# Kernel tuning notes

Hardware: AMD Instinct MI355X
Metric: run time of the kernel (lower is better)

The kernel has to match this reference:

```python
import math
import jax, jax.numpy as jnp
import numpy as np

NUM_HEADS = 8
ALPHA = 20.0
LN_EPS = 1e-5


def setup_inputs() -> dict:
    key = jax.random.key(0)
    ks = jax.random.split(key, 6)
    B, N, C = 8, 4096, 512
    s = 1.0 / math.sqrt(C)
    return {
        "x": jax.random.normal(ks[0], (B, N, C), dtype=jnp.float32),
        "qkv_w": jax.random.normal(ks[1], (C, 3 * C), dtype=jnp.float32) * s,
        "qkv_b": jnp.zeros((3 * C,), dtype=jnp.float32),
        "ln_g": jnp.ones((C,), dtype=jnp.float32),
        "ln_b": jnp.zeros((C,), dtype=jnp.float32),
        "out_w": jax.random.normal(ks[2], (C, C), dtype=jnp.float32) * s,
        "out_b": jnp.zeros((C,), dtype=jnp.float32),
    }


def _forward(x, qkv_w, qkv_b, ln_g, ln_b, out_w, out_b):
    B, N, C = x.shape
    H = NUM_HEADS
    D = C // H
    qkv = x @ qkv_w + qkv_b  # (B,N,3C)
    q, k, v = jnp.split(qkv, 3, axis=-1)

    def to_heads(t):
        return t.reshape(B, N, H, D).transpose(0, 2, 1, 3)  # (B,H,N,D)

    q, k, v = to_heads(q), to_heads(k), to_heads(v)

    # cosine-inhibit feature maps
    q_norm = jnp.linalg.norm(q, axis=-1, keepdims=True)  # (B,H,N,1)
    k_norm = jnp.linalg.norm(k, axis=-1, keepdims=True)
    q_t = q / q_norm
    dq = jnp.tanh(q / q_norm * ALPHA) * (math.pi / 4)
    dk = jnp.tanh(k / k_norm * ALPHA) * (math.pi / 4)
    k3 = jnp.abs(k) ** 3
    kf = jnp.concatenate([k3 * jnp.cos(dk), k3 * jnp.sin(dk)], axis=-1)  # (B,H,N,2D)
    power = 1.5 * (0.5 + jnp.tanh(q_norm))
    q_t = (q_t ** 2) ** power
    qf = jnp.concatenate([q_t * jnp.cos(dq), q_t * jnp.sin(dq)], axis=-1)  # (B,H,N,2D)

    # O(N) linear attention
    k_mean = jnp.mean(kf, axis=2, keepdims=True)  # (B,H,1,2D)
    z = 1.0 / (jnp.einsum('bhnf,bhmf->bhnm', qf, k_mean) + 1e-6)  # (B,H,N,1)
    scale = N ** (-0.5)
    kv = jnp.einsum('bhnf,bhnd->bhfd', kf * scale, v * scale)  # (B,H,2D,D)
    out = jnp.einsum('bhnf,bhfd->bhnd', qf, kv) * z  # (B,H,N,D)

    out = out.transpose(0, 2, 1, 3).reshape(B, N, C)
    # LayerNorm
    mu = jnp.mean(out, axis=-1, keepdims=True)
    var = jnp.var(out, axis=-1, keepdims=True)
    out = (out - mu) * jax.lax.rsqrt(var + LN_EPS) * ln_g + ln_b
    return out @ out_w + out_b


def reference(x, qkv_w, qkv_b, ln_g, ln_b, out_w, out_b):
    return _forward(x, qkv_w, qkv_b, ln_g, ln_b, out_w, out_b)
```

## Files before the change

### kernel.cpp

```cpp
#include <hip/hip_runtime.h>
#include <math.h>

#define Bb 8
#define Nn 4096
#define Cc 512
#define Hh 8
#define Dd 64
#define Ff 128
#define M_ROWS (Bb * Nn)
#define PI4f 0.78539816339744830962f
#define CHB 16
#define PART 8320

using bf16x8 = __attribute__((ext_vector_type(8))) short;
using f32x4 = __attribute__((ext_vector_type(4))) float;

__device__ __forceinline__ unsigned short f2bf(float f) {
  unsigned u = __float_as_uint(f);
  u += 0x7FFFu + ((u >> 16) & 1u);
  return (unsigned short)(u >> 16);
}
__device__ __forceinline__ float bf2f(unsigned short h) {
  return __uint_as_float(((unsigned)h) << 16);
}
__device__ __forceinline__ float grp16_sum(float v) {
  v += __shfl_xor(v, 1);
  v += __shfl_xor(v, 2);
  v += __shfl_xor(v, 4);
  v += __shfl_xor(v, 8);
  return v;
}
__device__ __forceinline__ float wsum64(float v) {
#pragma unroll
  for (int m = 32; m >= 1; m >>= 1) v += __shfl_xor(v, m, 64);
  return v;
}
__device__ __forceinline__ float fast_tanh(float x) {
  float e = __expf(2.0f * x);
  return 1.0f - 2.0f / (e + 1.0f);
}

__global__ __launch_bounds__(256) void x_convert(const float* __restrict__ x,
                                                 unsigned short* __restrict__ xb) {
  size_t i = ((size_t)blockIdx.x * 256 + threadIdx.x) * 8;
  float4 a = *(const float4*)(x + i);
  float4 b = *(const float4*)(x + i + 4);
  int4 o;
  o.x = (int)f2bf(a.x) | ((int)f2bf(a.y) << 16);
  o.y = (int)f2bf(a.z) | ((int)f2bf(a.w) << 16);
  o.z = (int)f2bf(b.x) | ((int)f2bf(b.y) << 16);
  o.w = (int)f2bf(b.z) | ((int)f2bf(b.w) << 16);
  *(int4*)(xb + i) = o;
}

__global__ __launch_bounds__(256) void w_transpose(const float* __restrict__ qkvw,
                                                   const float* __restrict__ outw,
                                                   unsigned short* __restrict__ wt,
                                                   unsigned short* __restrict__ owt) {
  __shared__ float tile[64][65];
  const int bid = blockIdx.x;
  const float* src;
  unsigned short* dst;
  int ldsrc, j0, k0;
  if (bid < 192) {
    src = qkvw; dst = wt; ldsrc = 1536;
    j0 = (bid % 24) * 64; k0 = (bid / 24) * 64;
  } else {
    int r = bid - 192;
    src = outw; dst = owt; ldsrc = 512;
    j0 = (r & 7) * 64; k0 = (r >> 3) * 64;
  }
  const int t = threadIdx.x;
  const int rr = t >> 4, cc = (t & 15) * 4;
#pragma unroll
  for (int it = 0; it < 4; ++it) {
    float4 v = *(const float4*)(src + (size_t)(k0 + rr + it * 16) * ldsrc + j0 + cc);
    tile[rr + it * 16][cc + 0] = v.x;
    tile[rr + it * 16][cc + 1] = v.y;
    tile[rr + it * 16][cc + 2] = v.z;
    tile[rr + it * 16][cc + 3] = v.w;
  }
  __syncthreads();
  const int j = t >> 2, kq = (t & 3) * 16;
  unsigned short u[16];
#pragma unroll
  for (int p = 0; p < 16; ++p) u[p] = f2bf(tile[kq + p][j]);
  int4 o;
  o.x = (int)u[0] | ((int)u[1] << 16);
  o.y = (int)u[2] | ((int)u[3] << 16);
  o.z = (int)u[4] | ((int)u[5] << 16);
  o.w = (int)u[6] | ((int)u[7] << 16);
  int4 o2;
  o2.x = (int)u[8] | ((int)u[9] << 16);
  o2.y = (int)u[10] | ((int)u[11] << 16);
  o2.z = (int)u[12] | ((int)u[13] << 16);
  o2.w = (int)u[14] | ((int)u[15] << 16);
  *(int4*)(dst + (size_t)(j0 + j) * 512 + k0 + kq) = o;
  *(int4*)(dst + (size_t)(j0 + j) * 512 + k0 + kq + 8) = o2;
}

__global__ __launch_bounds__(256) void kv_kernel(const unsigned short* __restrict__ xb,
                                                 const unsigned short* __restrict__ wt,
                                                 const float* __restrict__ qkvb,
                                                 float* __restrict__ part) {
  __shared__ char smraw[54272];
  unsigned short* As = (unsigned short*)smraw;
  unsigned short* Bs = As + 128 * 72;
  unsigned short* kf_t = (unsigned short*)smraw;
  unsigned short* v_t = kf_t + 128 * 136;
  float* ksl = (float*)(smraw + 52224);
  const int t = threadIdx.x, lane = t & 63, wv = t >> 6;
  const int i = lane & 15, g = lane >> 4, kq = g * 8;
  const int bh = blockIdx.x >> 4, chunk = blockIdx.x & 15;
  const int b = bh >> 3, h = bh & 7;
  const int sr = t >> 1, sko = (t & 1) * 32;
  const int wrow = (sr < 64) ? (512 + h * 64 + sr) : (1024 + h * 64 + sr - 64);
  const unsigned short* bg = wt + (size_t)wrow * 512 + sko;
  float bias_[8];
#pragma unroll
  for (int ni = 0; ni < 4; ++ni) bias_[ni] = qkvb[512 + h * 64 + 16 * ni + i];
#pragma unroll
  for (int ni = 4; ni < 8; ++ni) bias_[ni] = qkvb[1024 + h * 64 + 16 * (ni - 4) + i];
  f32x4 kvf[2][4] = {};
  float ksc[4] = {0.f, 0.f, 0.f, 0.f}, kss[4] = {0.f, 0.f, 0.f, 0.f};
  const size_t rowbase = (size_t)b * Nn + chunk * 256;
  const unsigned short* ag0 = xb + (rowbase + sr) * 512 + sko;
  bf16x8 pa[4], pb[4];
#pragma unroll
  for (int p = 0; p < 4; ++p) {
    pa[p] = *(const bf16x8*)(ag0 + p * 8);
    pb[p] = *(const bf16x8*)(bg + p * 8);
  }
  for (int t2 = 0; t2 < 2; ++t2) {
    const unsigned short* ag = xb + (rowbase + t2 * 128 + sr) * 512 + sko;
    f32x4 acc[2][8] = {};
    for (int k0 = 0; k0 < 512; k0 += 64) {
      __syncthreads();
#pragma unroll
      for (int p = 0; p < 4; ++p) {
        *(bf16x8*)&As[sr * 72 + sko + p * 8] = pa[p];
        *(bf16x8*)&Bs[sr * 72 + sko + p * 8] = pb[p];
      }
      __syncthreads();
      if (k0 < 448) {
#pragma unroll
        for (int p = 0; p < 4; ++p) {
          pa[p] = *(const bf16x8*)(ag + k0 + 64 + p * 8);
          pb[p] = *(const bf16x8*)(bg + k0 + 64 + p * 8);
        }
      } else if (t2 == 0) {
        const unsigned short* ag1 = ag + 128 * 512;
#pragma unroll
        for (int p = 0; p < 4; ++p) {
          pa[p] = *(const bf16x8*)(ag1 + p * 8);
          pb[p] = *(const bf16x8*)(bg + p * 8);
        }
      }
#pragma unroll
      for (int ks = 0; ks < 2; ++ks) {
        bf16x8 am[2], bn[8];
#pragma unroll
        for (int mi = 0; mi < 2; ++mi)
          am[mi] = *(const bf16x8*)&As[(32 * wv + 16 * mi + i) * 72 + ks * 32 + kq];
#pragma unroll
        for (int ni = 0; ni < 8; ++ni)
          bn[ni] = *(const bf16x8*)&Bs[(16 * ni + i) * 72 + ks * 32 + kq];
#pragma unroll
        for (int mi = 0; mi < 2; ++mi)
#pragma unroll
          for (int ni = 0; ni < 8; ++ni)
            acc[mi][ni] = __builtin_amdgcn_mfma_f32_16x16x32_bf16(am[mi], bn[ni], acc[mi][ni], 0, 0, 0);
      }
    }
    __syncthreads();
#pragma unroll
    for (int mi = 0; mi < 2; ++mi) {
      float nrm[4];
#pragma unroll
      for (int r = 0; r < 4; ++r) {
        float s = 0.f;
#pragma unroll
        for (int ni = 0; ni < 4; ++ni) {
          float kx = acc[mi][ni][r] + bias_[ni];
          s += kx * kx;
        }
        nrm[r] = sqrtf(grp16_sum(s));
      }
#pragma unroll
      for (int ni = 0; ni < 4; ++ni)
#pragma unroll
        for (int r = 0; r < 4; ++r) {
          float kx = acc[mi][ni][r] + bias_[ni];
          float dk = fast_tanh(kx / nrm[r] * 20.0f) * PI4f;
          float a3 = fabsf(kx);
          a3 = a3 * a3 * a3;
          float sn, cs;
          __sincosf(dk, &sn, &cs);
          float kc = a3 * cs, ksn = a3 * sn;
          ksc[ni] += kc;
          kss[ni] += ksn;
          const int nl = 32 * wv + 16 * mi + 4 * g + r;
          kf_t[(16 * ni + i) * 136 + nl] = f2bf(kc);
          kf_t[(64 + 16 * ni + i) * 136 + nl] = f2bf(ksn);
        }
#pragma unroll
      for (int ni = 4; ni < 8; ++ni)
#pragma unroll
        for (int r = 0; r < 4; ++r) {
          const int nl = 32 * wv + 16 * mi + 4 * g + r;
          v_t[(16 * (ni - 4) + i) * 136 + nl] = f2bf(acc[mi][ni][r] + bias_[ni]);
        }
    }
    __syncthreads();
#pragma unroll
    for (int ks2 = 0; ks2 < 4; ++ks2) {
      bf16x8 a2[2], b2[4];
#pragma unroll
      for (int mi = 0; mi < 2; ++mi)
        a2[mi] = *(const bf16x8*)&kf_t[(32 * wv + 16 * mi + i) * 136 + ks2 * 32 + kq];
#pragma unroll
      for (int ni = 0; ni < 4; ++ni)
        b2[ni] = *(const bf16x8*)&v_t[(16 * ni + i) * 136 + ks2 * 32 + kq];
#pragma unroll
      for (int mi = 0; mi < 2; ++mi)
#pragma unroll
        for (int ni = 0; ni < 4; ++ni)
          kvf[mi][ni] = __builtin_amdgcn_mfma_f32_16x16x32_bf16(a2[mi], b2[ni], kvf[mi][ni], 0, 0, 0);
    }
  }
  float* pw = part + (size_t)blockIdx.x * PART;
#pragma unroll
  for (int mi = 0; mi < 2; ++mi)
#pragma unroll
    for (int ni = 0; ni < 4; ++ni)
#pragma unroll
      for (int r = 0; r < 4; ++r)
        pw[(32 * wv + 16 * mi + 4 * g + r) * 64 + 16 * ni + i] = kvf[mi][ni][r];
#pragma unroll
  for (int ni = 0; ni < 4; ++ni) {
    float c = ksc[ni];
    c += __shfl_xor(c, 16);
    c += __shfl_xor(c, 32);
    float s = kss[ni];
    s += __shfl_xor(s, 16);
    s += __shfl_xor(s, 32);
    if (lane < 16) {
      ksl[wv * 128 + 16 * ni + lane] = c;
      ksl[wv * 128 + 64 + 16 * ni + lane] = s;
    }
  }
  __syncthreads();
  if (t < 128) pw[8192 + t] = ksl[t] + ksl[128 + t] + ksl[256 + t] + ksl[384 + t];
}

__global__ __launch_bounds__(256) void kv_reduce(const float* __restrict__ part,
                                                 unsigned short* __restrict__ kvt,
                                                 float* __restrict__ kmean) {
  const int bh = blockIdx.x;
  const float invN = 1.0f / Nn;
  const size_t base = (size_t)bh * CHB * PART;
  for (int idx = threadIdx.x; idx < 8192; idx += 256) {
    float s = 0.f;
#pragma unroll
    for (int c = 0; c < CHB; ++c) s += part[base + (size_t)c * PART + idx];
    int f = idx >> 6, d = idx & 63;
    kvt[(size_t)bh * 8192 + d * 128 + f] = f2bf(s * invN);
  }
  if (threadIdx.x < 128) {
    float s = 0.f;
#pragma unroll
    for (int c = 0; c < CHB; ++c) s += part[base + (size_t)c * PART + 8192 + threadIdx.x];
    kmean[bh * 128 + threadIdx.x] = s * invN;
  }
}

__global__ __launch_bounds__(256) void attn_kernel(const unsigned short* __restrict__ xb,
                                                   const unsigned short* __restrict__ wt,
                                                   const float* __restrict__ qkvb,
                                                   const unsigned short* __restrict__ kvt,
                                                   const float* __restrict__ kmean,
                                                   unsigned short* __restrict__ attb) {
  __shared__ char smraw[52736];
  unsigned short* As = (unsigned short*)smraw;
  unsigned short* Bs = As + 128 * 72;
  unsigned short* qf_t = (unsigned short*)smraw;
  unsigned short* kv_s = (unsigned short*)(smraw + 34816);
  float* km = (float*)(smraw + 34816 + 17408);
  const int t = threadIdx.x, lane = t & 63, wv = t >> 6;
  const int i = lane & 15, g = lane >> 4, kq = g * 8;
  const int bh = blockIdx.x >> 5, chunk = blockIdx.x & 31;
  const int b = bh >> 3, h = bh & 7;
  const size_t row0 = (size_t)b * Nn + chunk * 128;
  if (t < 128) km[t] = kmean[bh * 128 + t];
  {
    const unsigned short* src = kvt + (size_t)bh * 8192;
#pragma unroll
    for (int it = 0; it < 4; ++it) {
      int idx = t + it * 256;
      int d = idx >> 4, f8 = (idx & 15) * 8;
      *(bf16x8*)&kv_s[d * 136 + f8] = *(const bf16x8*)(src + d * 128 + f8);
    }
  }
  const int sr = t >> 1, sko = (t & 1) * 32;
  const int c2 = t >> 2, ko2 = (t & 3) * 16;
  const unsigned short* ag = xb + (row0 + sr) * 512 + sko;
  const unsigned short* bgq = wt + (size_t)(h * 64 + c2) * 512 + ko2;
  bf16x8 pa[4], pb[2];
#pragma unroll
  for (int p = 0; p < 4; ++p) pa[p] = *(const bf16x8*)(ag + p * 8);
#pragma unroll
  for (int p = 0; p < 2; ++p) pb[p] = *(const bf16x8*)(bgq + p * 8);
  f32x4 acc[2][4] = {};
  for (int k0 = 0; k0 < 512; k0 += 64) {
    __syncthreads();
#pragma unroll
    for (int p = 0; p < 4; ++p) *(bf16x8*)&As[sr * 72 + sko + p * 8] = pa[p];
#pragma unroll
    for (int p = 0; p < 2; ++p) *(bf16x8*)&Bs[c2 * 72 + ko2 + p * 8] = pb[p];
    __syncthreads();
    if (k0 < 448) {
#pragma unroll
      for (int p = 0; p < 4; ++p) pa[p] = *(const bf16x8*)(ag + k0 + 64 + p * 8);
#pragma unroll
      for (int p = 0; p < 2; ++p) pb[p] = *(const bf16x8*)(bgq + k0 + 64 + p * 8);
    }
#pragma unroll
    for (int ks = 0; ks < 2; ++ks) {
      bf16x8 am[2], bn[4];
#pragma unroll
      for (int mi = 0; mi < 2; ++mi)
        am[mi] = *(const bf16x8*)&As[(32 * wv + 16 * mi + i) * 72 + ks * 32 + kq];
#pragma unroll
      for (int ni = 0; ni < 4; ++ni)
        bn[ni] = *(const bf16x8*)&Bs[(16 * ni + i) * 72 + ks * 32 + kq];
#pragma unroll
      for (int mi = 0; mi < 2; ++mi)
#pragma unroll
        for (int ni = 0; ni < 4; ++ni)
          acc[mi][ni] = __builtin_amdgcn_mfma_f32_16x16x32_bf16(am[mi], bn[ni], acc[mi][ni], 0, 0, 0);
    }
  }
  __syncthreads();
  float bqv[4];
#pragma unroll
  for (int ni = 0; ni < 4; ++ni) bqv[ni] = qkvb[h * 64 + 16 * ni + i];
  float z[2][4];
#pragma unroll
  for (int mi = 0; mi < 2; ++mi) {
    float nrm[4];
#pragma unroll
    for (int r = 0; r < 4; ++r) {
      float s = 0.f;
#pragma unroll
      for (int ni = 0; ni < 4; ++ni) {
        float q = acc[mi][ni][r] + bqv[ni];
        s += q * q;
      }
      nrm[r] = sqrtf(grp16_sum(s));
    }
#pragma unroll
    for (int r = 0; r < 4; ++r) {
      float pwr = 1.5f * (0.5f + fast_tanh(nrm[r]));
      float dp = 0.f;
      const int nl = 32 * wv + 16 * mi + 4 * g + r;
#pragma unroll
      for (int ni = 0; ni < 4; ++ni) {
        float q = acc[mi][ni][r] + bqv[ni];
        float qt = q / nrm[r];
        float dq = fast_tanh(qt * 20.0f) * PI4f;
        float qtp = exp2f(pwr * __log2f(qt * qt));
        float sn, cs;
        __sincosf(dq, &sn, &cs);
        float qc = qtp * cs, qs = qtp * sn;
        dp += qc * km[16 * ni + i] + qs * km[64 + 16 * ni + i];
        qf_t[nl * 136 + 16 * ni + i] = f2bf(qc);
        qf_t[nl * 136 + 64 + 16 * ni + i] = f2bf(qs);
      }
      z[mi][r] = 1.0f / (grp16_sum(dp) + 1e-6f);
    }
  }
  __syncthreads();
  f32x4 pacc[2][4] = {};
#pragma unroll
  for (int ks2 = 0; ks2 < 4; ++ks2) {
    bf16x8 a2[2], b2[4];
#pragma unroll
    for (int mi = 0; mi < 2; ++mi)
      a2[mi] = *(const bf16x8*)&qf_t[(32 * wv + 16 * mi + i) * 136 + ks2 * 32 + kq];
#pragma unroll
    for (int ni = 0; ni < 4; ++ni)
      b2[ni] = *(const bf16x8*)&kv_s[(16 * ni + i) * 136 + ks2 * 32 + kq];
#pragma unroll
    for (int mi = 0; mi < 2; ++mi)
#pragma unroll
      for (int ni = 0; ni < 4; ++ni)
        pacc[mi][ni] = __builtin_amdgcn_mfma_f32_16x16x32_bf16(a2[mi], b2[ni], pacc[mi][ni], 0, 0, 0);
  }
#pragma unroll
  for (int mi = 0; mi < 2; ++mi)
#pragma unroll
    for (int ni = 0; ni < 4; ++ni)
#pragma unroll
      for (int r = 0; r < 4; ++r)
        attb[(row0 + 32 * wv + 16 * mi + 4 * g + r) * 512 + h * 64 + 16 * ni + i] =
            f2bf(pacc[mi][ni][r] * z[mi][r]);
}

__global__ __launch_bounds__(256) void ln_kernel(unsigned short* __restrict__ attb,
                                                 const float* __restrict__ gg,
                                                 const float* __restrict__ bb) {
  const int lane = threadIdx.x & 63, wv = threadIdx.x >> 6;
  const size_t row = (size_t)blockIdx.x * 4 + wv;
  unsigned short* p = attb + row * 512 + lane * 8;
  bf16x8 v = *(bf16x8*)p;
  float x[8];
#pragma unroll
  for (int j = 0; j < 8; ++j) x[j] = bf2f((unsigned short)v[j]);
  float s = 0.f;
#pragma unroll
  for (int j = 0; j < 8; ++j) s += x[j];
  const float mu = wsum64(s) * (1.0f / 512.0f);
  float sq = 0.f;
#pragma unroll
  for (int j = 0; j < 8; ++j) {
    float d = x[j] - mu;
    sq += d * d;
  }
  const float rstd = rsqrtf(wsum64(sq) * (1.0f / 512.0f) + 1e-5f);
  const float4 g0 = *(const float4*)(gg + lane * 8);
  const float4 g1 = *(const float4*)(gg + lane * 8 + 4);
  const float4 b0 = *(const float4*)(bb + lane * 8);
  const float4 b1 = *(const float4*)(bb + lane * 8 + 4);
  float gv[8] = {g0.x, g0.y, g0.z, g0.w, g1.x, g1.y, g1.z, g1.w};
  float bv[8] = {b0.x, b0.y, b0.z, b0.w, b1.x, b1.y, b1.z, b1.w};
#pragma unroll
  for (int j = 0; j < 8; ++j)
    v[j] = (short)f2bf((x[j] - mu) * rstd * gv[j] + bv[j]);
  *(bf16x8*)p = v;
}

__global__ __launch_bounds__(256) void out_gemm(const unsigned short* __restrict__ attb,
                                                const unsigned short* __restrict__ owt,
                                                const float* __restrict__ ob,
                                                float* __restrict__ outp) {
  __shared__ unsigned short As[128 * 72];
  __shared__ unsigned short Bs[128 * 72];
  const int t = threadIdx.x, lane = t & 63, wv = t >> 6;
  const int i = lane & 15, g = lane >> 4, kq = g * 8;
  const int wm = wv >> 1, wn = wv & 1;
  const int m0 = (blockIdx.x >> 2) * 128, n0 = (blockIdx.x & 3) * 128;
  const int sr = t >> 1, sko = (t & 1) * 32;
  const unsigned short* ag = attb + (size_t)(m0 + sr) * 512 + sko;
  const unsigned short* bg = owt + (size_t)(n0 + sr) * 512 + sko;
  f32x4 acc[4][4] = {};
  bf16x8 pa[4], pb[4];
#pragma unroll
  for (int p = 0; p < 4; ++p) {
    pa[p] = *(const bf16x8*)(ag + p * 8);
    pb[p] = *(const bf16x8*)(bg + p * 8);
  }
  for (int k0 = 0; k0 < 512; k0 += 64) {
    __syncthreads();
#pragma unroll
    for (int p = 0; p < 4; ++p) {
      *(bf16x8*)&As[sr * 72 + sko + p * 8] = pa[p];
      *(bf16x8*)&Bs[sr * 72 + sko + p * 8] = pb[p];
    }
    __syncthreads();
    if (k0 < 448) {
#pragma unroll
      for (int p = 0; p < 4; ++p) {
        pa[p] = *(const bf16x8*)(ag + k0 + 64 + p * 8);
        pb[p] = *(const bf16x8*)(bg + k0 + 64 + p * 8);
      }
    }
#pragma unroll
    for (int ks = 0; ks < 2; ++ks) {
      bf16x8 am[4], bn[4];
#pragma unroll
      for (int q = 0; q < 4; ++q) {
        am[q] = *(const bf16x8*)&As[(64 * wm + 16 * q + i) * 72 + ks * 32 + kq];
        bn[q] = *(const bf16x8*)&Bs[(64 * wn + 16 * q + i) * 72 + ks * 32 + kq];
      }
#pragma unroll
      for (int mi = 0; mi < 4; ++mi)
#pragma unroll
        for (int ni = 0; ni < 4; ++ni)
          acc[mi][ni] = __builtin_amdgcn_mfma_f32_16x16x32_bf16(am[mi], bn[ni], acc[mi][ni], 0, 0, 0);
    }
  }
#pragma unroll
  for (int ni = 0; ni < 4; ++ni) {
    float bv = ob[n0 + 64 * wn + 16 * ni + i];
#pragma unroll
    for (int mi = 0; mi < 4; ++mi)
#pragma unroll
      for (int r = 0; r < 4; ++r)
        outp[(size_t)(m0 + 64 * wm + 16 * mi + 4 * g + r) * 512 + n0 + 64 * wn +
             16 * ni + i] = acc[mi][ni][r] + bv;
  }
}

extern "C" void kernel_launch(void* const* d_in, const int* in_sizes, int n_in,
                              void* d_out, int out_size, void* d_ws,
                              size_t ws_size, hipStream_t stream) {
  const float* x = (const float*)d_in[0];
  const float* qkv_w = (const float*)d_in[1];
  const float* qkv_b = (const float*)d_in[2];
  const float* ln_g = (const float*)d_in[3];
  const float* ln_b = (const float*)d_in[4];
  const float* out_w = (const float*)d_in[5];
  const float* out_b = (const float*)d_in[6];
  float* out = (float*)d_out;

  char* w = (char*)d_ws;
  unsigned short* xb = (unsigned short*)w;
  unsigned short* wt = (unsigned short*)(w + 33554432);
  unsigned short* owt = (unsigned short*)(w + 35127296);
  unsigned short* kvt = (unsigned short*)(w + 35651584);
  float* kmean = (float*)(w + 36700160);
  char* R = w + 36732928;
  float* part = (float*)R;
  unsigned short* attb = (unsigned short*)R;

  x_convert<<<8192, 256, 0, stream>>>(x, xb);
  w_transpose<<<256, 256, 0, stream>>>(qkv_w, out_w, wt, owt);
  kv_kernel<<<1024, 256, 0, stream>>>(xb, wt, qkv_b, part);
  kv_reduce<<<64, 256, 0, stream>>>(part, kvt, kmean);
  attn_kernel<<<2048, 256, 0, stream>>>(xb, wt, qkv_b, kvt, kmean, attb);
  ln_kernel<<<8192, 256, 0, stream>>>(attb, ln_g, ln_b);
  out_gemm<<<1024, 256, 0, stream>>>(attb, owt, out_b, out);
}
```

Baseline: 357.8 us.

## Split QKV projection into standalone GEMM, use LDS direct loads and atomic KV reduction

Replaces the fused kv_kernel and attn_kernel, which each recomputed their share of the QKV projection, with one large qkv_gemm that writes a bf16 QKV buffer. The feature kernels then read from that buffer. The partial-sum buffer and kv_reduce kernel are dropped in favour of float atomicAdd into a zeroed accumulator. Both GEMMs switch to global_load_lds direct-to-LDS loads with an XCD-aware block swizzle. The cost is an extra round trip through a 100 MB bf16 intermediate, a memset, and loss of register prefetch double-buffering.

Measured after the change: 353.9 us. About the same (-1.1%).

```diff
diff --git a/kernel.cpp b/kernel.cpp
--- a/kernel.cpp
+++ b/kernel.cpp
@@ -5,12 +5,7 @@
 #define Nn 4096
 #define Cc 512
 #define Hh 8
-#define Dd 64
-#define Ff 128
-#define M_ROWS (Bb * Nn)
 #define PI4f 0.78539816339744830962f
-#define CHB 16
-#define PART 8320
 
 using bf16x8 = __attribute__((ext_vector_type(8))) short;
 using f32x4 = __attribute__((ext_vector_type(4))) float;
@@ -38,6 +33,11 @@
 __device__ __forceinline__ float fast_tanh(float x) {
   float e = __expf(2.0f * x);
   return 1.0f - 2.0f / (e + 1.0f);
+}
+__device__ __forceinline__ void gload16(const unsigned short* g, unsigned short* l) {
+  __builtin_amdgcn_global_load_lds(
+      (const __attribute__((address_space(1))) void*)g,
+      (__attribute__((address_space(3))) void*)l, 16, 0, 0);
 }
 
 __global__ __launch_bounds__(256) void x_convert(const float* __restrict__ x,
@@ -99,100 +99,101 @@
   *(int4*)(dst + (size_t)(j0 + j) * 512 + k0 + kq + 8) = o2;
 }
 
-__global__ __launch_bounds__(256) void kv_kernel(const unsigned short* __restrict__ xb,
-                                                 const unsigned short* __restrict__ wt,
-                                                 const float* __restrict__ qkvb,
-                                                 float* __restrict__ part) {
-  __shared__ char smraw[54272];
-  unsigned short* As = (unsigned short*)smraw;
-  unsigned short* Bs = As + 128 * 72;
-  unsigned short* kf_t = (unsigned short*)smraw;
-  unsigned short* v_t = kf_t + 128 * 136;
-  float* ksl = (float*)(smraw + 52224);
+__global__ __launch_bounds__(256) void qkv_gemm(const unsigned short* __restrict__ xb,
+                                                const unsigned short* __restrict__ wt,
+                                                const float* __restrict__ bias,
+                                                unsigned short* __restrict__ qkvb) {
+  __shared__ unsigned short As[128 * 64];
+  __shared__ unsigned short Bs[128 * 64];
   const int t = threadIdx.x, lane = t & 63, wv = t >> 6;
   const int i = lane & 15, g = lane >> 4, kq = g * 8;
-  const int bh = blockIdx.x >> 4, chunk = blockIdx.x & 15;
+  const int wm = wv >> 1, wn = wv & 1;
+  const int sbid = ((int)blockIdx.x & 7) * 384 + ((int)blockIdx.x >> 3);
+  const int mt = sbid / 12, nt = sbid - mt * 12;
+  const int m0 = mt * 128, n0 = nt * 128;
+  const int lrow = lane >> 3, lchunk = (lane & 7) * 8;
+  const unsigned short* agb = xb + (size_t)(m0 + 32 * wv + lrow) * 512 + lchunk;
+  const unsigned short* bgb = wt + (size_t)(n0 + 32 * wv + lrow) * 512 + lchunk;
+  unsigned short* asb = &As[(32 * wv) * 64];
+  unsigned short* bsb = &Bs[(32 * wv) * 64];
+  f32x4 acc[4][4] = {};
+  for (int k0 = 0; k0 < 512; k0 += 64) {
+    __syncthreads();
+#pragma unroll
+    for (int c = 0; c < 4; ++c) {
+      gload16(agb + (size_t)(8 * c) * 512 + k0, asb + 8 * c * 64);
+      gload16(bgb + (size_t)(8 * c) * 512 + k0, bsb + 8 * c * 64);
+    }
+    __syncthreads();
+#pragma unroll
+    for (int ks = 0; ks < 2; ++ks) {
+      bf16x8 am[4], bn[4];
+#pragma unroll
+      for (int q = 0; q < 4; ++q) {
+        am[q] = *(const bf16x8*)&As[(64 * wm + 16 * q + i) * 64 + ks * 32 + kq];
+        bn[q] = *(const bf16x8*)&Bs[(64 * wn + 16 * q + i) * 64 + ks * 32 + kq];
+      }
+#pragma unroll
+      for (int mi = 0; mi < 4; ++mi)
+#pragma unroll
+        for (int ni = 0; ni < 4; ++ni)
+          acc[mi][ni] = __builtin_amdgcn_mfma_f32_16x16x32_bf16(am[mi], bn[ni], acc[mi][ni], 0, 0, 0);
+    }
+  }
+#pragma unroll
+  for (int ni = 0; ni < 4; ++ni) {
+    const int col = n0 + 64 * wn + 16 * ni + i;
+    const float bv = bias[col];
+#pragma unroll
+    for (int mi = 0; mi < 4; ++mi) {
+      const size_t rowb = (size_t)(m0 + 64 * wm + 16 * mi + 4 * g) * 1536 + col;
+#pragma unroll
+      for (int r = 0; r < 4; ++r)
+        qkvb[rowb + (size_t)r * 1536] = f2bf(acc[mi][ni][r] + bv);
+    }
+  }
+}
+
+__global__ __launch_bounds__(256) void kv_feat(const unsigned short* __restrict__ qkvb,
+                                               float* __restrict__ kvacc,
+                                               float* __restrict__ ksum) {
+  __shared__ unsigned short kf_t[128 * 136];
+  __shared__ unsigned short v_t[64 * 136];
+  const int t = threadIdx.x, lane = t & 63, wv = t >> 6;
+  const int i = lane & 15, g = lane >> 4, kq = g * 8;
+  const int bh = (int)blockIdx.x >> 4, chunk = (int)blockIdx.x & 15;
   const int b = bh >> 3, h = bh & 7;
-  const int sr = t >> 1, sko = (t & 1) * 32;
-  const int wrow = (sr < 64) ? (512 + h * 64 + sr) : (1024 + h * 64 + sr - 64);
-  const unsigned short* bg = wt + (size_t)wrow * 512 + sko;
-  float bias_[8];
-#pragma unroll
-  for (int ni = 0; ni < 4; ++ni) bias_[ni] = qkvb[512 + h * 64 + 16 * ni + i];
-#pragma unroll
-  for (int ni = 4; ni < 8; ++ni) bias_[ni] = qkvb[1024 + h * 64 + 16 * (ni - 4) + i];
+  const size_t rowbase = (size_t)b * Nn + chunk * 256;
   f32x4 kvf[2][4] = {};
   float ksc[4] = {0.f, 0.f, 0.f, 0.f}, kss[4] = {0.f, 0.f, 0.f, 0.f};
-  const size_t rowbase = (size_t)b * Nn + chunk * 256;
-  const unsigned short* ag0 = xb + (rowbase + sr) * 512 + sko;
-  bf16x8 pa[4], pb[4];
-#pragma unroll
-  for (int p = 0; p < 4; ++p) {
-    pa[p] = *(const bf16x8*)(ag0 + p * 8);
-    pb[p] = *(const bf16x8*)(bg + p * 8);
-  }
   for (int t2 = 0; t2 < 2; ++t2) {
-    const unsigned short* ag = xb + (rowbase + t2 * 128 + sr) * 512 + sko;
-    f32x4 acc[2][8] = {};
-    for (int k0 = 0; k0 < 512; k0 += 64) {
-      __syncthreads();
-#pragma unroll
-      for (int p = 0; p < 4; ++p) {
-        *(bf16x8*)&As[sr * 72 + sko + p * 8] = pa[p];
-        *(bf16x8*)&Bs[sr * 72 + sko + p * 8] = pb[p];
-      }
-      __syncthreads();
-      if (k0 < 448) {
-#pragma unroll
-        for (int p = 0; p < 4; ++p) {
-          pa[p] = *(const bf16x8*)(ag + k0 + 64 + p * 8);
-          pb[p] = *(const bf16x8*)(bg + k0 + 64 + p * 8);
-        }
-      } else if (t2 == 0) {
-        const unsigned short* ag1 = ag + 128 * 512;
-#pragma unroll
-        for (int p = 0; p < 4; ++p) {
-          pa[p] = *(const bf16x8*)(ag1 + p * 8);
-          pb[p] = *(const bf16x8*)(bg + p * 8);
+#pragma unroll
+    for (int mi = 0; mi < 2; ++mi) {
+      float kx[4][4], vx[4][4];
+#pragma unroll
+      for (int r = 0; r < 4; ++r) {
+        const unsigned short* rp =
+            qkvb + (rowbase + t2 * 128 + 32 * wv + 16 * mi + 4 * g + r) * 1536 + h * 64 + i;
+#pragma unroll
+        for (int ni = 0; ni < 4; ++ni) {
+          kx[ni][r] = bf2f(rp[512 + 16 * ni]);
+          vx[ni][r] = bf2f(rp[1024 + 16 * ni]);
         }
       }
-#pragma unroll
-      for (int ks = 0; ks < 2; ++ks) {
-        bf16x8 am[2], bn[8];
-#pragma unroll
-        for (int mi = 0; mi < 2; ++mi)
-          am[mi] = *(const bf16x8*)&As[(32 * wv + 16 * mi + i) * 72 + ks * 32 + kq];
-#pragma unroll
-        for (int ni = 0; ni < 8; ++ni)
-          bn[ni] = *(const bf16x8*)&Bs[(16 * ni + i) * 72 + ks * 32 + kq];
-#pragma unroll
-        for (int mi = 0; mi < 2; ++mi)
-#pragma unroll
-          for (int ni = 0; ni < 8; ++ni)
-            acc[mi][ni] = __builtin_amdgcn_mfma_f32_16x16x32_bf16(am[mi], bn[ni], acc[mi][ni], 0, 0, 0);
-      }
-    }
-    __syncthreads();
-#pragma unroll
-    for (int mi = 0; mi < 2; ++mi) {
       float nrm[4];
 #pragma unroll
       for (int r = 0; r < 4; ++r) {
-        float s = 0.f;
-#pragma unroll
-        for (int ni = 0; ni < 4; ++ni) {
-          float kx = acc[mi][ni][r] + bias_[ni];
-          s += kx * kx;
-        }
+        float s = kx[0][r] * kx[0][r] + kx[1][r] * kx[1][r] +
+                  kx[2][r] * kx[2][r] + kx[3][r] * kx[3][r];
         nrm[r] = sqrtf(grp16_sum(s));
       }
 #pragma unroll
       for (int ni = 0; ni < 4; ++ni)
 #pragma unroll
         for (int r = 0; r < 4; ++r) {
-          float kx = acc[mi][ni][r] + bias_[ni];
-          float dk = fast_tanh(kx / nrm[r] * 20.0f) * PI4f;
-          float a3 = fabsf(kx);
+          float k1 = kx[ni][r];
+          float dk = fast_tanh(k1 / nrm[r] * 20.0f) * PI4f;
+          float a3 = fabsf(k1);
           a3 = a3 * a3 * a3;
           float sn, cs;
           __sincosf(dk, &sn, &cs);
@@ -202,13 +203,7 @@
           const int nl = 32 * wv + 16 * mi + 4 * g + r;
           kf_t[(16 * ni + i) * 136 + nl] = f2bf(kc);
           kf_t[(64 + 16 * ni + i) * 136 + nl] = f2bf(ksn);
-        }
-#pragma unroll
-      for (int ni = 4; ni < 8; ++ni)
-#pragma unroll
-        for (int r = 0; r < 4; ++r) {
-          const int nl = 32 * wv + 16 * mi + 4 * g + r;
-          v_t[(16 * (ni - 4) + i) * 136 + nl] = f2bf(acc[mi][ni][r] + bias_[ni]);
+          v_t[(16 * ni + i) * 136 + nl] = f2bf(vx[ni][r]);
         }
     }
     __syncthreads();
@@ -227,15 +222,17 @@
         for (int ni = 0; ni < 4; ++ni)
           kvf[mi][ni] = __builtin_amdgcn_mfma_f32_16x16x32_bf16(a2[mi], b2[ni], kvf[mi][ni], 0, 0, 0);
     }
-  }
-  float* pw = part + (size_t)blockIdx.x * PART;
+    __syncthreads();
+  }
 #pragma unroll
   for (int mi = 0; mi < 2; ++mi)
 #pragma unroll
     for (int ni = 0; ni < 4; ++ni)
 #pragma unroll
       for (int r = 0; r < 4; ++r)
-        pw[(32 * wv + 16 * mi + 4 * g + r) * 64 + 16 * ni + i] = kvf[mi][ni][r];
+        atomicAdd(kvacc + (size_t)bh * 8192 +
+                      (32 * wv + 16 * mi + 4 * g + r) * 64 + 16 * ni + i,
+                  kvf[mi][ni][r]);
 #pragma unroll
   for (int ni = 0; ni < 4; ++ni) {
     float c = ksc[ni];
@@ -245,117 +242,49 @@
     s += __shfl_xor(s, 16);
     s += __shfl_xor(s, 32);
     if (lane < 16) {
-      ksl[wv * 128 + 16 * ni + lane] = c;
-      ksl[wv * 128 + 64 + 16 * ni + lane] = s;
-    }
-  }
-  __syncthreads();
-  if (t < 128) pw[8192 + t] = ksl[t] + ksl[128 + t] + ksl[256 + t] + ksl[384 + t];
-}
-
-__global__ __launch_bounds__(256) void kv_reduce(const float* __restrict__ part,
-                                                 unsigned short* __restrict__ kvt,
-                                                 float* __restrict__ kmean) {
-  const int bh = blockIdx.x;
-  const float invN = 1.0f / Nn;
-  const size_t base = (size_t)bh * CHB * PART;
-  for (int idx = threadIdx.x; idx < 8192; idx += 256) {
-    float s = 0.f;
-#pragma unroll
-    for (int c = 0; c < CHB; ++c) s += part[base + (size_t)c * PART + idx];
-    int f = idx >> 6, d = idx & 63;
-    kvt[(size_t)bh * 8192 + d * 128 + f] = f2bf(s * invN);
-  }
-  if (threadIdx.x < 128) {
-    float s = 0.f;
-#pragma unroll
-    for (int c = 0; c < CHB; ++c) s += part[base + (size_t)c * PART + 8192 + threadIdx.x];
-    kmean[bh * 128 + threadIdx.x] = s * invN;
-  }
-}
-
-__global__ __launch_bounds__(256) void attn_kernel(const unsigned short* __restrict__ xb,
-                                                   const unsigned short* __restrict__ wt,
-                                                   const float* __restrict__ qkvb,
-                                                   const unsigned short* __restrict__ kvt,
-                                                   const float* __restrict__ kmean,
-                                                   unsigned short* __restrict__ attb) {
-  __shared__ char smraw[52736];
-  unsigned short* As = (unsigned short*)smraw;
-  unsigned short* Bs = As + 128 * 72;
-  unsigned short* qf_t = (unsigned short*)smraw;
-  unsigned short* kv_s = (unsigned short*)(smraw + 34816);
-  float* km = (float*)(smraw + 34816 + 17408);
+      atomicAdd(ksum + bh * 128 + 16 * ni + lane, c);
+      atomicAdd(ksum + bh * 128 + 64 + 16 * ni + lane, s);
+    }
+  }
+}
+
+__global__ __launch_bounds__(256) void attn_feat(const unsigned short* __restrict__ qkvb,
+                                                 const float* __restrict__ kvacc,
+                                                 const float* __restrict__ ksum,
+                                                 unsigned short* __restrict__ attb) {
+  __shared__ unsigned short qf_t[128 * 136];
+  __shared__ unsigned short kv_s[64 * 136];
+  __shared__ float km[128];
   const int t = threadIdx.x, lane = t & 63, wv = t >> 6;
   const int i = lane & 15, g = lane >> 4, kq = g * 8;
-  const int bh = blockIdx.x >> 5, chunk = blockIdx.x & 31;
+  const int bh = (int)blockIdx.x >> 5, chunk = (int)blockIdx.x & 31;
   const int b = bh >> 3, h = bh & 7;
   const size_t row0 = (size_t)b * Nn + chunk * 128;
-  if (t < 128) km[t] = kmean[bh * 128 + t];
-  {
-    const unsigned short* src = kvt + (size_t)bh * 8192;
-#pragma unroll
-    for (int it = 0; it < 4; ++it) {
-      int idx = t + it * 256;
-      int d = idx >> 4, f8 = (idx & 15) * 8;
-      *(bf16x8*)&kv_s[d * 136 + f8] = *(const bf16x8*)(src + d * 128 + f8);
-    }
-  }
-  const int sr = t >> 1, sko = (t & 1) * 32;
-  const int c2 = t >> 2, ko2 = (t & 3) * 16;
-  const unsigned short* ag = xb + (row0 + sr) * 512 + sko;
-  const unsigned short* bgq = wt + (size_t)(h * 64 + c2) * 512 + ko2;
-  bf16x8 pa[4], pb[2];
-#pragma unroll
-  for (int p = 0; p < 4; ++p) pa[p] = *(const bf16x8*)(ag + p * 8);
-#pragma unroll
-  for (int p = 0; p < 2; ++p) pb[p] = *(const bf16x8*)(bgq + p * 8);
-  f32x4 acc[2][4] = {};
-  for (int k0 = 0; k0 < 512; k0 += 64) {
-    __syncthreads();
-#pragma unroll
-    for (int p = 0; p < 4; ++p) *(bf16x8*)&As[sr * 72 + sko + p * 8] = pa[p];
-#pragma unroll
-    for (int p = 0; p < 2; ++p) *(bf16x8*)&Bs[c2 * 72 + ko2 + p * 8] = pb[p];
-    __syncthreads();
-    if (k0 < 448) {
-#pragma unroll
-      for (int p = 0; p < 4; ++p) pa[p] = *(const bf16x8*)(ag + k0 + 64 + p * 8);
-#pragma unroll
-      for (int p = 0; p < 2; ++p) pb[p] = *(const bf16x8*)(bgq + k0 + 64 + p * 8);
-    }
-#pragma unroll
-    for (int ks = 0; ks < 2; ++ks) {
-      bf16x8 am[2], bn[4];
-#pragma unroll
-      for (int mi = 0; mi < 2; ++mi)
-        am[mi] = *(const bf16x8*)&As[(32 * wv + 16 * mi + i) * 72 + ks * 32 + kq];
-#pragma unroll
-      for (int ni = 0; ni < 4; ++ni)
-        bn[ni] = *(const bf16x8*)&Bs[(16 * ni + i) * 72 + ks * 32 + kq];
-#pragma unroll
-      for (int mi = 0; mi < 2; ++mi)
-#pragma unroll
-        for (int ni = 0; ni < 4; ++ni)
-          acc[mi][ni] = __builtin_amdgcn_mfma_f32_16x16x32_bf16(am[mi], bn[ni], acc[mi][ni], 0, 0, 0);
-    }
-  }
+  const float invN = 1.0f / Nn;
+  for (int idx = t; idx < 8192; idx += 256) {
+    int f = idx >> 6, d = idx & 63;
+    kv_s[d * 136 + f] = f2bf(kvacc[(size_t)bh * 8192 + idx] * invN);
+  }
+  if (t < 128) km[t] = ksum[bh * 128 + t] * invN;
+  float qx[2][4][4];
+#pragma unroll
+  for (int mi = 0; mi < 2; ++mi)
+#pragma unroll
+    for (int r = 0; r < 4; ++r) {
+      const unsigned short* rp =
+          qkvb + (row0 + 32 * wv + 16 * mi + 4 * g + r) * 1536 + h * 64 + i;
+#pragma unroll
+      for (int ni = 0; ni < 4; ++ni) qx[mi][ni][r] = bf2f(rp[16 * ni]);
+    }
   __syncthreads();
-  float bqv[4];
-#pragma unroll
-  for (int ni = 0; ni < 4; ++ni) bqv[ni] = qkvb[h * 64 + 16 * ni + i];
   float z[2][4];
 #pragma unroll
   for (int mi = 0; mi < 2; ++mi) {
     float nrm[4];
 #pragma unroll
     for (int r = 0; r < 4; ++r) {
-      float s = 0.f;
-#pragma unroll
-      for (int ni = 0; ni < 4; ++ni) {
-        float q = acc[mi][ni][r] + bqv[ni];
-        s += q * q;
-      }
+      float s = qx[mi][0][r] * qx[mi][0][r] + qx[mi][1][r] * qx[mi][1][r] +
+                qx[mi][2][r] * qx[mi][2][r] + qx[mi][3][r] * qx[mi][3][r];
       nrm[r] = sqrtf(grp16_sum(s));
     }
 #pragma unroll
@@ -365,7 +294,7 @@
       const int nl = 32 * wv + 16 * mi + 4 * g + r;
 #pragma unroll
       for (int ni = 0; ni < 4; ++ni) {
-        float q = acc[mi][ni][r] + bqv[ni];
+        float q = qx[mi][ni][r];
         float qt = q / nrm[r];
         float dq = fast_tanh(qt * 20.0f) * PI4f;
         float qtp = exp2f(pwr * __log2f(qt * qt));
@@ -443,44 +372,34 @@
                                                 const unsigned short* __restrict__ owt,
                                                 const float* __restrict__ ob,
                                                 float* __restrict__ outp) {
-  __shared__ unsigned short As[128 * 72];
-  __shared__ unsigned short Bs[128 * 72];
+  __shared__ unsigned short As[128 * 64];
+  __shared__ unsigned short Bs[128 * 64];
   const int t = threadIdx.x, lane = t & 63, wv = t >> 6;
   const int i = lane & 15, g = lane >> 4, kq = g * 8;
   const int wm = wv >> 1, wn = wv & 1;
-  const int m0 = (blockIdx.x >> 2) * 128, n0 = (blockIdx.x & 3) * 128;
-  const int sr = t >> 1, sko = (t & 1) * 32;
-  const unsigned short* ag = attb + (size_t)(m0 + sr) * 512 + sko;
-  const unsigned short* bg = owt + (size_t)(n0 + sr) * 512 + sko;
+  const int sbid = ((int)blockIdx.x & 7) * 128 + ((int)blockIdx.x >> 3);
+  const int m0 = (sbid >> 2) * 128, n0 = (sbid & 3) * 128;
+  const int lrow = lane >> 3, lchunk = (lane & 7) * 8;
+  const unsigned short* agb = attb + (size_t)(m0 + 32 * wv + lrow) * 512 + lchunk;
+  const unsigned short* bgb = owt + (size_t)(n0 + 32 * wv + lrow) * 512 + lchunk;
+  unsigned short* asb = &As[(32 * wv) * 64];
+  unsigned short* bsb = &Bs[(32 * wv) * 64];
   f32x4 acc[4][4] = {};
-  bf16x8 pa[4], pb[4];
-#pragma unroll
-  for (int p = 0; p < 4; ++p) {
-    pa[p] = *(const bf16x8*)(ag + p * 8);
-    pb[p] = *(const bf16x8*)(bg + p * 8);
-  }
   for (int k0 = 0; k0 < 512; k0 += 64) {
     __syncthreads();
 #pragma unroll
-    for (int p = 0; p < 4; ++p) {
-      *(bf16x8*)&As[sr * 72 + sko + p * 8] = pa[p];
-      *(bf16x8*)&Bs[sr * 72 + sko + p * 8] = pb[p];
-    }
-    __syncthreads();
-    if (k0 < 448) {
-#pragma unroll
-      for (int p = 0; p < 4; ++p) {
-        pa[p] = *(const bf16x8*)(ag + k0 + 64 + p * 8);
-        pb[p] = *(const bf16x8*)(bg + k0 + 64 + p * 8);
-      }
-    }
+    for (int c = 0; c < 4; ++c) {
+      gload16(agb + (size_t)(8 * c) * 512 + k0, asb + 8 * c * 64);
+      gload16(bgb + (size_t)(8 * c) * 512 + k0, bsb + 8 * c * 64);
+    }
+    __syncthreads();
 #pragma unroll
     for (int ks = 0; ks < 2; ++ks) {
       bf16x8 am[4], bn[4];
 #pragma unroll
       for (int q = 0; q < 4; ++q) {
-        am[q] = *(const bf16x8*)&As[(64 * wm + 16 * q + i) * 72 + ks * 32 + kq];
-        bn[q] = *(const bf16x8*)&Bs[(64 * wn + 16 * q + i) * 72 + ks * 32 + kq];
+        am[q] = *(const bf16x8*)&As[(64 * wm + 16 * q + i) * 64 + ks * 32 + kq];
+        bn[q] = *(const bf16x8*)&Bs[(64 * wn + 16 * q + i) * 64 + ks * 32 + kq];
       }
 #pragma unroll
       for (int mi = 0; mi < 4; ++mi)
@@ -491,7 +410,7 @@
   }
 #pragma unroll
   for (int ni = 0; ni < 4; ++ni) {
-    float bv = ob[n0 + 64 * wn + 16 * ni + i];
+    const float bv = ob[n0 + 64 * wn + 16 * ni + i];
 #pragma unroll
     for (int mi = 0; mi < 4; ++mi)
 #pragma unroll
@@ -515,19 +434,19 @@
 
   char* w = (char*)d_ws;
   unsigned short* xb = (unsigned short*)w;
+  unsigned short* attb = xb;
   unsigned short* wt = (unsigned short*)(w + 33554432);
   unsigned short* owt = (unsigned short*)(w + 35127296);
-  unsigned short* kvt = (unsigned short*)(w + 35651584);
-  float* kmean = (float*)(w + 36700160);
-  char* R = w + 36732928;
-  float* part = (float*)R;
-  unsigned short* attb = (unsigned short*)R;
-
+  float* kvacc = (float*)(w + 35651584);
+  float* ksum = (float*)(w + 37748736);
+  unsigned short* qkvb = (unsigned short*)(w + 37781504);
+
+  hipMemsetAsync(kvacc, 0, 2097152 + 32768, stream);
   x_convert<<<8192, 256, 0, stream>>>(x, xb);
   w_transpose<<<256, 256, 0, stream>>>(qkv_w, out_w, wt, owt);
-  kv_kernel<<<1024, 256, 0, stream>>>(xb, wt, qkv_b, part);
-  kv_reduce<<<64, 256, 0, stream>>>(part, kvt, kmean);
-  attn_kernel<<<2048, 256, 0, stream>>>(xb, wt, qkv_b, kvt, kmean, attb);
+  qkv_gemm<<<3072, 256, 0, stream>>>(xb, wt, qkv_b, qkvb);
+  kv_feat<<<1024, 256, 0, stream>>>(qkvb, kvacc, ksum);
+  attn_feat<<<2048, 256, 0, stream>>>(qkvb, kvacc, ksum, attb);
   ln_kernel<<<8192, 256, 0, stream>>>(attb, ln_g, ln_b);
   out_gemm<<<1024, 256, 0, stream>>>(attb, owt, out_b, out);
 }
```
